# Kernel optimization log

Measured on AMD Instinct MI355X. Metric: run time of the kernel, lower is better.

The kernel has to match this reference:

```python
import jax, jax.numpy as jnp
import numpy as np

# Static hyperparams matching init_kwargs
KSIZE, STRIDE, PAD, DIL = 3, 2, 1, 1


def setup_inputs() -> dict:
    key = jax.random.key(0)
    k1, k2 = jax.random.split(key)
    B, H, W, Cin, Cout = 8, 128, 128, 128, 256
    feats = jax.random.normal(k1, (B * H * W, Cin), dtype=jnp.float32)
    weight = jax.random.normal(k2, (KSIZE * KSIZE, Cin, Cout), dtype=jnp.float32) * 0.05
    alpha_upper = jnp.ones((1,), dtype=jnp.float32)
    # dense grid coords [N, 3] = (batch, y, x), matching a dense image sparse tensor
    bb, yy, xx = np.meshgrid(np.arange(B), np.arange(H), np.arange(W), indexing='ij')
    coords = jnp.asarray(np.stack([bb, yy, xx], -1).reshape(-1, 3), dtype=jnp.int32)
    return {"feats": feats, "weight": weight, "alpha_upper": alpha_upper,
            "coords": coords, "H": H, "W": W, "B": B}


def _coord_ranges(H, W):
    # Faithful translation of WrappedMinkowskiStridedOperation.__init__ + forward
    # coordinate math, specialized to a dense grid (per-batch min=0, max=H-1/W-1).
    kernel_origin = DIL * ((KSIZE - 1) // 2) * (KSIZE % 2)
    dilated = DIL * (KSIZE - 1) + 1
    ks_off = kernel_origin - dilated + 1          # _kernel_start_offset
    ke_off = kernel_origin                        # _kernel_end_offset
    idx_start = kernel_origin - PAD               # _index_start_offset
    ranges = []
    for ext in (H, W):
        idx_end = (ext - 1) + kernel_origin + PAD - dilated + 2
        start = max(idx_start, (0 + ks_off - idx_start) // STRIDE * STRIDE + idx_start)
        end = min(idx_end, ((ext - 1 + ke_off - idx_start) // STRIDE + 1) * STRIDE + idx_start)
        ranges.append(np.arange(start, end, STRIDE))
    offsets = np.arange(KSIZE) * DIL - kernel_origin  # kernel region offsets
    return ranges[0], ranges[1], offsets, idx_start


def reference(feats, weight, alpha_upper, coords, H, W, B):
    Cin = feats.shape[1]
    Cout = weight.shape[-1]
    ys, xs, offs, idx_start = _coord_ranges(H, W)
    OH, OW = len(ys), len(xs)
    oy, ox = jnp.meshgrid(jnp.asarray(ys, jnp.int32), jnp.asarray(xs, jnp.int32), indexing='ij')
    dy, dx = np.meshgrid(offs, offs, indexing='ij')
    dy = jnp.asarray(dy.reshape(-1), jnp.int32)  # [kvol]
    dx = jnp.asarray(dx.reshape(-1), jnp.int32)
    ny = oy[None] + dy[:, None, None]            # [kvol, OH, OW]
    nx = ox[None] + dx[:, None, None]
    valid = (ny >= 0) & (ny < H) & (nx >= 0) & (nx < W)
    lin = jnp.clip(ny, 0, H - 1) * W + jnp.clip(nx, 0, W - 1)  # [kvol, OH, OW]
    feats3 = feats.reshape(B, H * W, Cin)
    gathered = feats3[:, lin]                    # [B, kvol, OH, OW, Cin]
    gathered = jnp.where(valid[None, ..., None], gathered, jnp.zeros((), feats.dtype))
    out = jnp.einsum('bkhwc,kcd->bhwd', gathered, weight)  # [B, OH, OW, Cout]
    out_feats = out.reshape(B * OH * OW, Cout)
    # output coordinates, remapped as in forward (shift by index_start, divide by stride)
    oc = jnp.stack([oy, ox], -1).reshape(-1, 2)  # [OH*OW, 2]
    oc = (oc - jnp.int32(idx_start)) // jnp.int32(STRIDE)
    oc = jnp.tile(oc, (B, 1))
    bcol = jnp.repeat(jnp.arange(B, dtype=jnp.int32), OH * OW)
    out_coords = jnp.concatenate([bcol[:, None], oc], axis=1)
    return out_feats, out_coords, alpha_upper
```

## Files before the change

### kernel.cpp

```cpp
#include <hip/hip_runtime.h>


#define OUT_FEATS_ELEMS (32768 * 256)
#define OUT_COORDS_OFF  OUT_FEATS_ELEMS
#define ALPHA_OFF       (OUT_FEATS_ELEMS + 32768 * 3)

#define F8_BYTES   16777216
#define BW_BYTES   (18 * 16384)
#define ZP_OFF     (F8_BYTES + BW_BYTES)

typedef float v16f __attribute__((ext_vector_type(16)));

__device__ __forceinline__ unsigned pk4fp8(float a, float b, float c, float d) {
    unsigned u = 0;
    u = __builtin_amdgcn_cvt_pk_fp8_f32(a, b, u, false);
    u = __builtin_amdgcn_cvt_pk_fp8_f32(c, d, u, true);
    return u;
}

#define GLOAD_LDS16(SRC, DST)                                                  \
    __builtin_amdgcn_global_load_lds(                                          \
        (const __attribute__((address_space(1))) void*)(SRC),                  \
        (__attribute__((address_space(3))) void*)(DST), 16, 0, 0)

__global__ void prep_kernel(const float* __restrict__ feats, const float* __restrict__ w,
                            const float* __restrict__ alpha,
                            unsigned char* __restrict__ F8, unsigned char* __restrict__ Bw,
                            float* __restrict__ out) {
    int bid = blockIdx.x;
    if (bid < 8192) {
        int i = bid * 256 + threadIdx.x;
        const float4* f = (const float4*)feats;
        float4 a = f[2 * i];
        float4 b = f[2 * i + 1];
        uint2 r;
        r.x = pk4fp8(a.x, a.y, a.z, a.w);
        r.y = pk4fp8(b.x, b.y, b.z, b.w);
        ((uint2*)F8)[i] = r;
        return;
    }
    int cid = (bid - 8192) * 256 + threadIdx.x;
    if (cid < 32768) {
        int b = cid >> 12, iy = (cid >> 6) & 63, ix = cid & 63;
        float* c = out + OUT_COORDS_OFF + (size_t)cid * 3;
        c[0] = (float)b; c[1] = (float)iy; c[2] = (float)ix;
        if (cid == 0) out[ALPHA_OFF] = alpha[0];
    }
    if (cid < 8) {
        uint4 z; z.x = 0u; z.y = 0u; z.z = 0u; z.w = 0u;
        *(uint4*)(Bw + BW_BYTES + cid * 16) = z;
    }
    if (cid < 18432) {
        int ch  = cid & 7;
        int row = (cid >> 3) & 127;
        int t   = cid >> 10;
        int nb  = (t >= 9) ? 1 : 0;
        int tap = t - 9 * nb;
        int chp = ch ^ (row & 7);
        int n   = (nb << 7) + row;
        int kb  = (tap << 7) + (chp << 4);
        unsigned u[4];
#pragma unroll
        for (int q = 0; q < 4; ++q) {
            float f0 = w[(size_t)(kb + 4 * q + 0) * 256 + n];
            float f1 = w[(size_t)(kb + 4 * q + 1) * 256 + n];
            float f2 = w[(size_t)(kb + 4 * q + 2) * 256 + n];
            float f3 = w[(size_t)(kb + 4 * q + 3) * 256 + n];
            u[q] = pk4fp8(f0, f1, f2, f3);
        }
        uint4 r; r.x = u[0]; r.y = u[1]; r.z = u[2]; r.w = u[3];
        *(uint4*)(Bw + (size_t)cid * 16) = r;
    }
}

__global__ void coords_alpha_kernel(float* __restrict__ out, const float* __restrict__ alpha) {
    int i = blockIdx.x * 256 + threadIdx.x;
    int b = i >> 12, iy = (i >> 6) & 63, ix = i & 63;
    float* c = out + OUT_COORDS_OFF + (size_t)i * 3;
    c[0] = (float)b; c[1] = (float)iy; c[2] = (float)ix;
    if (i == 0) out[ALPHA_OFF] = alpha[0];
}

__global__ __launch_bounds__(512, 2) void gemm_conv_kernel(
    const unsigned char* __restrict__ F8,
    const unsigned char* __restrict__ Bw,
    float* __restrict__ out)
{
    __shared__ unsigned char At[3][128 * 128];
    __shared__ unsigned char Bs[3][256 * 128];

    const int tid  = threadIdx.x;
    const int bid  = blockIdx.x;
    const int my   = ((bid & 7) << 5) + (bid >> 3);
    const int m0   = my << 7;
    const int bb   = my >> 5;
    const int iy0  = (my << 1) & 63;

    const int lane = tid & 63, wave = tid >> 6;
    const int wm   = (wave >> 2) << 6;
    const int wn   = (wave & 3) << 6;
    const int l31  = lane & 31;
    const int hh   = lane >> 5;
    const int xorl = l31 & 7;

    const int srow = lane >> 3;
    const int chp  = (lane & 7) ^ srow;
    const long rowA0 = (long)bb << 14;
    const unsigned char* zp = Bw + BW_BYTES;
    const unsigned char* bsrc0 = Bw + ((size_t)((wave >> 2) * 9) << 14)
                                    + ((size_t)(wave & 3) << 12) + ((size_t)lane << 4);

    v16f acc[2][2];
#pragma unroll
    for (int i = 0; i < 2; i++)
#pragma unroll
        for (int j = 0; j < 2; j++) acc[i][j] = (v16f)(0.0f);

    auto stage = [&](int tap, int buf) {
        const int dy = tap / 3 - 1;
        const int dx = tap % 3 - 1;
        const unsigned char* bs = bsrc0 + ((size_t)tap << 14);
        unsigned char* bdst = Bs[buf] + (wave << 12);
#pragma unroll
        for (int q = 0; q < 4; ++q)
            GLOAD_LDS16(bs + (q << 10), bdst + (q << 10));
        unsigned char* adst = At[buf] + (wave << 11);
#pragma unroll
        for (int it = 0; it < 2; ++it) {
            const int region = (wave << 1) + it;
            const int row = (region << 3) + srow;
            const int iyl = region >> 3;
            const int ny  = ((iy0 + iyl) << 1) + dy;
            const int nx  = ((row & 63) << 1) + dx;
            const unsigned char* asrc =
                (((unsigned)ny < 128u) & ((unsigned)nx < 128u))
                    ? F8 + ((rowA0 + ((long)ny << 7) + nx) << 7) + (chp << 4)
                    : zp + (chp << 4);
            GLOAD_LDS16(asrc, adst + (it << 10));
        }
    };

    auto compute = [&](int buf) {
#pragma unroll
        for (int seg = 0; seg < 8; ++seg) {
            const int q = seg ^ xorl;
            long long a[2], b2[2];
#pragma unroll
            for (int i = 0; i < 2; i++)
                a[i] = *(const long long*)(At[buf] + ((wm + (i << 5) + l31) << 7) + (q << 4) + (hh << 3));
#pragma unroll
            for (int j = 0; j < 2; j++)
                b2[j] = *(const long long*)(Bs[buf] + ((wn + (j << 5) + l31) << 7) + (q << 4) + (hh << 3));
            __builtin_amdgcn_s_setprio(1);
#pragma unroll
            for (int i = 0; i < 2; i++)
#pragma unroll
                for (int j = 0; j < 2; j++)
                    acc[i][j] = __builtin_amdgcn_mfma_f32_32x32x16_fp8_fp8(a[i], b2[j], acc[i][j], 0, 0, 0);
            __builtin_amdgcn_s_setprio(0);
        }
    };

    stage(0, 0);
    stage(1, 1);

#pragma unroll
    for (int tap = 0; tap < 9; ++tap) {
        const int buf = tap % 3;
        if (tap < 7) {
            stage(tap + 2, (tap + 2) % 3);
            asm volatile("s_waitcnt vmcnt(12)\ns_barrier" ::: "memory");
        } else if (tap == 7) {
            asm volatile("s_waitcnt vmcnt(6)\ns_barrier" ::: "memory");
        } else {
            asm volatile("s_waitcnt vmcnt(0)\ns_barrier" ::: "memory");
        }
        compute(tap == 8 ? 2 : buf);
        asm volatile("s_barrier" ::: "memory");
    }

#pragma unroll
    for (int i = 0; i < 2; i++)
#pragma unroll
        for (int j = 0; j < 2; j++) {
            const int gcol = wn + (j << 5) + l31;
#pragma unroll
            for (int r = 0; r < 16; ++r) {
                const int grow = m0 + wm + (i << 5) + (r & 3) + ((r >> 2) << 3) + (hh << 2);
                __builtin_nontemporal_store(acc[i][j][r], &out[(size_t)grow * 256 + gcol]);
            }
        }
}

__global__ void naive_conv_kernel(const float* __restrict__ feats,
                                  const float* __restrict__ w,
                                  float* __restrict__ out) {
    int m = blockIdx.x;
    int n = threadIdx.x;
    int bb = m >> 12, iy = (m >> 6) & 63, ix = m & 63;
    float acc = 0.f;
    for (int tap = 0; tap < 9; ++tap) {
        int ny = 2 * iy + tap / 3 - 1;
        int nx = 2 * ix + tap % 3 - 1;
        if ((unsigned)ny < 128u && (unsigned)nx < 128u) {
            const float* fr = feats + ((size_t)((bb << 14) + (ny << 7) + nx) << 7);
            const float* wr = w + tap * 32768 + n;
            for (int c = 0; c < 128; ++c) acc += fr[c] * wr[c * 256];
        }
    }
    out[(size_t)m * 256 + n] = acc;
}

extern "C" void kernel_launch(void* const* d_in, const int* in_sizes, int n_in,
                              void* d_out, int out_size, void* d_ws, size_t ws_size,
                              hipStream_t stream) {
    const float* feats  = (const float*)d_in[0];
    const float* weight = (const float*)d_in[1];
    const float* alpha  = (const float*)d_in[2];
    float* out = (float*)d_out;

    const size_t NEED = (size_t)F8_BYTES + BW_BYTES + 128;
    if (ws_size >= NEED) {
        unsigned char* F8 = (unsigned char*)d_ws;
        unsigned char* Bw = F8 + F8_BYTES;
        prep_kernel<<<8336, 256, 0, stream>>>(feats, weight, alpha, F8, Bw, out);
        gemm_conv_kernel<<<256, 512, 0, stream>>>(F8, Bw, out);
    } else {
        coords_alpha_kernel<<<128, 256, 0, stream>>>(out, alpha);
        naive_conv_kernel<<<32768, 256, 0, stream>>>(feats, weight, out);
    }
}
```

Baseline: 135.9 us.

## Fuse fp8 feature conversion into conv kernel with shared input band

Drops the separate pass that converts all input features to fp8 in workspace. Each conv block now loads its fp32 input row band (5 rows × 130 padded columns) directly, converts it to fp8 into a swizzled LDS band, and reuses that band across all 9 taps instead of gathering A per tap. Only the weights are double-buffered now, and launch bounds drop to 1 block per CU because LDS use grows. This removes one full read/write of the features and the per-tap A loads. In exchange, the fp32 band load is not overlapped with compute and occupancy is lower.

```diff
diff --git a/kernel.cpp b/kernel.cpp
--- a/kernel.cpp
+++ b/kernel.cpp
@@ -5,9 +5,7 @@
 #define OUT_COORDS_OFF  OUT_FEATS_ELEMS
 #define ALPHA_OFF       (OUT_FEATS_ELEMS + 32768 * 3)
 
-#define F8_BYTES   16777216
 #define BW_BYTES   (18 * 16384)
-#define ZP_OFF     (F8_BYTES + BW_BYTES)
 
 typedef float v16f __attribute__((ext_vector_type(16)));
 
@@ -23,32 +21,16 @@
         (const __attribute__((address_space(1))) void*)(SRC),                  \
         (__attribute__((address_space(3))) void*)(DST), 16, 0, 0)
 
-__global__ void prep_kernel(const float* __restrict__ feats, const float* __restrict__ w,
-                            const float* __restrict__ alpha,
-                            unsigned char* __restrict__ F8, unsigned char* __restrict__ Bw,
-                            float* __restrict__ out) {
-    int bid = blockIdx.x;
-    if (bid < 8192) {
-        int i = bid * 256 + threadIdx.x;
-        const float4* f = (const float4*)feats;
-        float4 a = f[2 * i];
-        float4 b = f[2 * i + 1];
-        uint2 r;
-        r.x = pk4fp8(a.x, a.y, a.z, a.w);
-        r.y = pk4fp8(b.x, b.y, b.z, b.w);
-        ((uint2*)F8)[i] = r;
-        return;
-    }
-    int cid = (bid - 8192) * 256 + threadIdx.x;
+__global__ void wprep_kernel(const float* __restrict__ w,
+                             const float* __restrict__ alpha,
+                             unsigned char* __restrict__ Bw,
+                             float* __restrict__ out) {
+    int cid = blockIdx.x * 256 + threadIdx.x;
     if (cid < 32768) {
         int b = cid >> 12, iy = (cid >> 6) & 63, ix = cid & 63;
         float* c = out + OUT_COORDS_OFF + (size_t)cid * 3;
         c[0] = (float)b; c[1] = (float)iy; c[2] = (float)ix;
         if (cid == 0) out[ALPHA_OFF] = alpha[0];
-    }
-    if (cid < 8) {
-        uint4 z; z.x = 0u; z.y = 0u; z.z = 0u; z.w = 0u;
-        *(uint4*)(Bw + BW_BYTES + cid * 16) = z;
     }
     if (cid < 18432) {
         int ch  = cid & 7;
@@ -81,20 +63,20 @@
     if (i == 0) out[ALPHA_OFF] = alpha[0];
 }
 
-__global__ __launch_bounds__(512, 2) void gemm_conv_kernel(
-    const unsigned char* __restrict__ F8,
+__global__ __launch_bounds__(512, 1) void gemm_conv_kernel(
+    const float* __restrict__ feats,
     const unsigned char* __restrict__ Bw,
     float* __restrict__ out)
 {
-    __shared__ unsigned char At[3][128 * 128];
-    __shared__ unsigned char Bs[3][256 * 128];
+    __shared__ unsigned char Aband[5 * 130 * 128];
+    __shared__ unsigned char Bs[2][256 * 128];
 
     const int tid  = threadIdx.x;
     const int bid  = blockIdx.x;
     const int my   = ((bid & 7) << 5) + (bid >> 3);
     const int m0   = my << 7;
     const int bb   = my >> 5;
-    const int iy0  = (my << 1) & 63;
+    const int iy0  = ((my & 31) << 1);
 
     const int lane = tid & 63, wave = tid >> 6;
     const int wm   = (wave >> 2) << 6;
@@ -103,54 +85,76 @@
     const int hh   = lane >> 5;
     const int xorl = l31 & 7;
 
-    const int srow = lane >> 3;
-    const int chp  = (lane & 7) ^ srow;
-    const long rowA0 = (long)bb << 14;
-    const unsigned char* zp = Bw + BW_BYTES;
+    if (tid < 40) {
+        const int r = tid >> 3, c = tid & 7;
+        uint4 z; z.x = 0u; z.y = 0u; z.z = 0u; z.w = 0u;
+        *(uint4*)(Aband + ((r * 130) << 7) + (c << 4)) = z;
+    }
+    if (iy0 == 0) {
+        for (int z = tid; z < 1040; z += 512) {
+            const int nxp = z >> 3, c = z & 7;
+            uint4 zz; zz.x = 0u; zz.y = 0u; zz.z = 0u; zz.w = 0u;
+            *(uint4*)(Aband + (nxp << 7) + ((c ^ ((nxp >> 1) & 7)) << 4)) = zz;
+        }
+    }
+
+    {
+        const int vstart = (iy0 == 0) ? 1 : 0;
+        const int iters  = (5 - vstart) << 3;
+        const int ny0    = (iy0 << 1) - 1;
+        for (int it = 0; it < iters; ++it) {
+            const int o   = (tid + (it << 9)) << 4;
+            const int r   = vstart + (o >> 16);
+            const int br  = o & 65535;
+            const int nx  = br >> 9;
+            const int ch0 = (br & 511) >> 2;
+            const float4 f = *(const float4*)(feats +
+                ((((size_t)(bb << 14) + (ny0 + r) * 128 + nx)) << 7) + ch0);
+            const unsigned u = pk4fp8(f.x, f.y, f.z, f.w);
+            const int c   = ch0 >> 4;
+            const int nxp = nx + 1;
+            *(unsigned*)(Aband + ((r * 130 + nxp) << 7)
+                         + ((c ^ ((nxp >> 1) & 7)) << 4) + (ch0 & 15)) = u;
+        }
+    }
+    __syncthreads();
+
     const unsigned char* bsrc0 = Bw + ((size_t)((wave >> 2) * 9) << 14)
                                     + ((size_t)(wave & 3) << 12) + ((size_t)lane << 4);
-
-    v16f acc[2][2];
-#pragma unroll
-    for (int i = 0; i < 2; i++)
-#pragma unroll
-        for (int j = 0; j < 2; j++) acc[i][j] = (v16f)(0.0f);
-
-    auto stage = [&](int tap, int buf) {
-        const int dy = tap / 3 - 1;
-        const int dx = tap % 3 - 1;
+    auto stageB = [&](int tap, int buf) {
         const unsigned char* bs = bsrc0 + ((size_t)tap << 14);
         unsigned char* bdst = Bs[buf] + (wave << 12);
 #pragma unroll
         for (int q = 0; q < 4; ++q)
             GLOAD_LDS16(bs + (q << 10), bdst + (q << 10));
-        unsigned char* adst = At[buf] + (wave << 11);
-#pragma unroll
-        for (int it = 0; it < 2; ++it) {
-            const int region = (wave << 1) + it;
-            const int row = (region << 3) + srow;
-            const int iyl = region >> 3;
-            const int ny  = ((iy0 + iyl) << 1) + dy;
-            const int nx  = ((row & 63) << 1) + dx;
-            const unsigned char* asrc =
-                (((unsigned)ny < 128u) & ((unsigned)nx < 128u))
-                    ? F8 + ((rowA0 + ((long)ny << 7) + nx) << 7) + (chp << 4)
-                    : zp + (chp << 4);
-            GLOAD_LDS16(asrc, adst + (it << 10));
-        }
     };
 
-    auto compute = [&](int buf) {
+    v16f acc[2][2];
+#pragma unroll
+    for (int i = 0; i < 2; i++)
+#pragma unroll
+        for (int j = 0; j < 2; j++) acc[i][j] = (v16f)(0.0f);
+
+    auto computeTap = [&](int buf, int dy, int dx) {
+        const int bandrow = (wm >> 5) + dy + 1;
+        int abase[2], akey[2];
+#pragma unroll
+        for (int i = 0; i < 2; ++i) {
+            const int ixv = (i << 5) + l31;
+            const int nxp = (ixv << 1) + dx + 1;
+            abase[i] = ((bandrow * 130 + nxp) << 7) + (hh << 3);
+            akey[i]  = (nxp >> 1) & 7;
+        }
 #pragma unroll
         for (int seg = 0; seg < 8; ++seg) {
-            const int q = seg ^ xorl;
             long long a[2], b2[2];
 #pragma unroll
             for (int i = 0; i < 2; i++)
-                a[i] = *(const long long*)(At[buf] + ((wm + (i << 5) + l31) << 7) + (q << 4) + (hh << 3));
+                a[i] = *(const long long*)(Aband + abase[i] + ((seg ^ akey[i]) << 4));
 #pragma unroll
             for (int j = 0; j < 2; j++)
-                b2[j] = *(const long long*)(Bs[buf] + ((wn + (j << 5) + l31) << 7) + (q << 4) + (hh << 3));
+                b2[j] = *(const long long*)(Bs[buf] + ((wn + (j << 5) + l31) << 7)
+                                            + ((seg ^ xorl) << 4) + (hh << 3));
             __builtin_amdgcn_s_setprio(1);
 #pragma unroll
             for (int i = 0; i < 2; i++)
@@ -161,22 +165,19 @@
         }
     };
 
-    stage(0, 0);
-    stage(1, 1);
+    stageB(0, 0);
 
 #pragma unroll
     for (int tap = 0; tap < 9; ++tap) {
-        const int buf = tap % 3;
-        if (tap < 7) {
-            stage(tap + 2, (tap + 2) % 3);
-            asm volatile("s_waitcnt vmcnt(12)\ns_barrier" ::: "memory");
-        } else if (tap == 7) {
-            asm volatile("s_waitcnt vmcnt(6)\ns_barrier" ::: "memory");
+        if (tap < 8) {
+            stageB(tap + 1, (tap + 1) & 1);
+            asm volatile("s_waitcnt vmcnt(4)\ns_barrier" ::: "memory");
         } else {
             asm volatile("s_waitcnt vmcnt(0)\ns_barrier" ::: "memory");
         }
-        compute(tap == 8 ? 2 : buf);
-        asm volatile("s_barrier" ::: "memory");
+        computeTap(tap & 1, tap / 3 - 1, tap % 3 - 1);
+        if (tap < 8)
+            asm volatile("s_barrier" ::: "memory");
     }
 
 #pragma unroll
@@ -219,12 +220,11 @@
     const float* alpha  = (const float*)d_in[2];
     float* out = (float*)d_out;
 
-    const size_t NEED = (size_t)F8_BYTES + BW_BYTES + 128;
+    const size_t NEED = (size_t)BW_BYTES;
     if (ws_size >= NEED) {
-        unsigned char* F8 = (unsigned char*)d_ws;
-        unsigned char* Bw = F8 + F8_BYTES;
-        prep_kernel<<<8336, 256, 0, stream>>>(feats, weight, alpha, F8, Bw, out);
-        gemm_conv_kernel<<<256, 512, 0, stream>>>(F8, Bw, out);
+        unsigned char* Bw = (unsigned char*)d_ws;
+        wprep_kernel<<<144, 256, 0, stream>>>(weight, alpha, Bw, out);
+        gemm_conv_kernel<<<256, 512, 0, stream>>>(feats, Bw, out);
     } else {
         coords_alpha_kernel<<<128, 256, 0, stream>>>(out, alpha);
         naive_conv_kernel<<<32768, 256, 0, stream>>>(feats, weight, out);
```

After: 132.4 us. -2.6%, faster.
